# Performance work log

Hardware: AMD Instinct MI355X
Metric: run time of the kernel (lower is better)

The kernel has to match this reference:

```python
import jax, jax.numpy as jnp
import numpy as np

N_NODES = 50000
N_EDGES = 800000
D = 256
N_LAYERS = 3
BN_EPS = 1e-5


def setup_inputs() -> dict:
    key = jax.random.key(0)
    ks = jax.random.split(key, 7)
    x = jax.random.normal(ks[0], (N_NODES, D), dtype=jnp.float32)
    Wl = jax.random.normal(ks[1], (N_LAYERS, D, D), dtype=jnp.float32)
    bl = jax.random.normal(ks[2], (N_LAYERS, D), dtype=jnp.float32)
    Wr = jax.random.normal(ks[3], (N_LAYERS, D, D), dtype=jnp.float32)
    gamma = jax.random.uniform(ks[4], (N_LAYERS, D), dtype=jnp.float32)
    beta = jax.random.normal(ks[5], (N_LAYERS, D), dtype=jnp.float32)
    edge_index = jax.random.randint(ks[6], (2, N_EDGES), 0, N_NODES, dtype=jnp.int64)
    return {"x": x, "Wl": Wl, "bl": bl, "Wr": Wr, "gamma": gamma,
            "beta": beta, "edge_index": edge_index}


def reference(x, Wl, bl, Wr, gamma, beta, edge_index):
    """3-layer GNN: SAGEConv(mean) -> BatchNorm1d(train) -> ReLU per layer."""
    src = edge_index[0]
    dst = edge_index[1]
    n = x.shape[0]
    # In-degree (mean-aggregation denominator); clamp to avoid div-by-zero.
    deg = jax.ops.segment_sum(jnp.ones((src.shape[0],), dtype=x.dtype), dst,
                              num_segments=n)
    deg = jnp.maximum(deg, 1.0)[:, None]  # [N, 1]
    n_layers = Wl.shape[0]
    for i in range(n_layers):
        # --- SAGEConv: mean-aggregate neighbor messages, then linear ---
        agg = jax.ops.segment_sum(x[src], dst, num_segments=n) / deg  # [N, D]
        h = agg @ Wl[i] + bl[i] + x @ Wr[i]                           # [N, D]
        # --- BatchNorm1d (training mode: batch stats, biased variance) ---
        mu = jnp.mean(h, axis=0)
        var = jnp.mean(jnp.square(h - mu), axis=0)
        h = (h - mu) * jax.lax.rsqrt(var + BN_EPS) * gamma[i] + beta[i]
        # --- ReLU ---
        x = jax.nn.relu(h)
    return x
```

## Files before the change

### kernel.cpp

```cpp
#include <hip/hip_runtime.h>

#define N_NODES 50000
#define N_PAD   50176
#define N_EDGES 800000
#define DIM     256
#define KDIM    512
#define BN_EPS  1e-5f
#define SCAN_NB ((N_NODES + 1023) / 1024)

typedef __attribute__((ext_vector_type(8))) short short8;
typedef __attribute__((ext_vector_type(4))) float floatx4;

__device__ __forceinline__ float bf2f(unsigned short u) {
    return __uint_as_float(((unsigned int)u) << 16);
}
__device__ __forceinline__ unsigned short f2bf(float f) {
    unsigned int b = __float_as_uint(f);
    b = (b + 0x7FFF + ((b >> 16) & 1)) >> 16;
    return (unsigned short)b;
}

__device__ __forceinline__ void gload_lds16(const void* g, void* l) {
    __builtin_amdgcn_global_load_lds(
        (const __attribute__((address_space(1))) unsigned int*)g,
        (__attribute__((address_space(3))) unsigned int*)l, 16, 0, 0);
}


__global__ void k_deg_count(const int* __restrict__ dst, int* __restrict__ degi) {
    int e = blockIdx.x * blockDim.x + threadIdx.x;
    if (e < N_EDGES) atomicAdd(&degi[dst[e]], 1);
}

__global__ void k_scan1(const int* __restrict__ degi, int* __restrict__ off,
                        float* __restrict__ inv_deg, int* __restrict__ bsums) {
    __shared__ int buf[1024];
    int i = blockIdx.x * 1024 + threadIdx.x;
    int v = (i < N_NODES) ? degi[i] : 0;
    if (i < N_NODES) inv_deg[i] = 1.0f / (float)max(v, 1);
    buf[threadIdx.x] = v;
    __syncthreads();
    for (int s = 1; s < 1024; s <<= 1) {
        int t = (threadIdx.x >= s) ? buf[threadIdx.x - s] : 0;
        __syncthreads();
        buf[threadIdx.x] += t;
        __syncthreads();
    }
    if (i < N_NODES) off[i + 1] = buf[threadIdx.x];
    if (threadIdx.x == 1023) bsums[blockIdx.x] = buf[1023];
    if (i == 0) off[0] = 0;
}

__global__ void k_scan2(int* __restrict__ bsums) {
    int t = threadIdx.x;
    int orig = (t < SCAN_NB) ? bsums[t] : 0;
    int v = orig;
    for (int s = 1; s < 64; s <<= 1) {
        int u = __shfl_up(v, s, 64);
        if (t >= s) v += u;
    }
    if (t < SCAN_NB) bsums[t] = v - orig;
}

__global__ void k_scan3(int* __restrict__ off, const int* __restrict__ bsums) {
    int i = blockIdx.x * 1024 + threadIdx.x;
    if (i < N_NODES) off[i + 1] += bsums[blockIdx.x];
}

__global__ void k_fill(const int* __restrict__ src, const int* __restrict__ dst,
                       const int* __restrict__ off, int* __restrict__ cursor,
                       int* __restrict__ csr_src) {
    int e = blockIdx.x * blockDim.x + threadIdx.x;
    if (e < N_EDGES) {
        int d = dst[e];
        int pos = atomicAdd(&cursor[d], 1);
        csr_src[off[d] + pos] = src[e];
    }
}


__global__ void k_prep_w(const float* __restrict__ Wl, const float* __restrict__ Wr,
                         unsigned short* __restrict__ Wcat) {
    int gid = blockIdx.x * blockDim.x + threadIdx.x;
    if (gid >= 3 * DIM * KDIM) return;
    int k = gid & (KDIM - 1);
    int n = (gid >> 9) & (DIM - 1);
    int l = gid >> 17;
    float v = (k < DIM) ? Wl[(size_t)l * DIM * DIM + (size_t)k * DIM + n]
                        : Wr[(size_t)l * DIM * DIM + (size_t)(k - DIM) * DIM + n];
    Wcat[gid] = f2bf(v);
}


__global__ void k_x2bf(const float* __restrict__ x, unsigned short* __restrict__ Acat) {
    size_t i = (size_t)blockIdx.x * blockDim.x + threadIdx.x;
    if (i >= (size_t)N_NODES * (DIM / 4)) return;
    int node = (int)(i >> 6);
    int c = ((int)i & 63) * 4;
    float4 v = ((const float4*)x)[i];
    ushort4 o; o.x = f2bf(v.x); o.y = f2bf(v.y); o.z = f2bf(v.z); o.w = f2bf(v.w);
    *(ushort4*)&Acat[(size_t)node * KDIM + DIM + c] = o;
}


__device__ __forceinline__ void addv(float* a, uint4 v) {
    unsigned int w[4] = {v.x, v.y, v.z, v.w};
    #pragma unroll
    for (int q = 0; q < 4; ++q) {
        a[2 * q + 0] += bf2f((unsigned short)(w[q] & 0xFFFF));
        a[2 * q + 1] += bf2f((unsigned short)(w[q] >> 16));
    }
}

__global__ __launch_bounds__(256) void k_aggregate(
        const unsigned short* __restrict__ Acat_x,
        const int* __restrict__ off,
        const int* __restrict__ csr_src,
        const float* __restrict__ inv_deg,
        unsigned short* __restrict__ Acat_agg) {
    int gid = blockIdx.x * blockDim.x + threadIdx.x;
    int node = gid >> 5;
    int lane = threadIdx.x & 31;
    if (node >= N_NODES) return;
    int beg = off[node], end = off[node + 1];
    float a[8];
    #pragma unroll
    for (int q = 0; q < 8; ++q) a[q] = 0.f;
    const unsigned short* xb = Acat_x + DIM + lane * 8;

    int e = beg;
    for (; e + 8 <= end; e += 8) {
        uint4 v0 = *(const uint4*)(xb + (size_t)csr_src[e + 0] * KDIM);
        uint4 v1 = *(const uint4*)(xb + (size_t)csr_src[e + 1] * KDIM);
        uint4 v2 = *(const uint4*)(xb + (size_t)csr_src[e + 2] * KDIM);
        uint4 v3 = *(const uint4*)(xb + (size_t)csr_src[e + 3] * KDIM);
        uint4 v4 = *(const uint4*)(xb + (size_t)csr_src[e + 4] * KDIM);
        uint4 v5 = *(const uint4*)(xb + (size_t)csr_src[e + 5] * KDIM);
        uint4 v6 = *(const uint4*)(xb + (size_t)csr_src[e + 6] * KDIM);
        uint4 v7 = *(const uint4*)(xb + (size_t)csr_src[e + 7] * KDIM);
        addv(a, v0); addv(a, v1); addv(a, v2); addv(a, v3);
        addv(a, v4); addv(a, v5); addv(a, v6); addv(a, v7);
    }
    for (; e + 4 <= end; e += 4) {
        uint4 v0 = *(const uint4*)(xb + (size_t)csr_src[e + 0] * KDIM);
        uint4 v1 = *(const uint4*)(xb + (size_t)csr_src[e + 1] * KDIM);
        uint4 v2 = *(const uint4*)(xb + (size_t)csr_src[e + 2] * KDIM);
        uint4 v3 = *(const uint4*)(xb + (size_t)csr_src[e + 3] * KDIM);
        addv(a, v0); addv(a, v1); addv(a, v2); addv(a, v3);
    }
    for (; e < end; ++e) {
        uint4 v = *(const uint4*)(xb + (size_t)csr_src[e] * KDIM);
        addv(a, v);
    }

    float inv = inv_deg[node];
    unsigned int w[4];
    #pragma unroll
    for (int q = 0; q < 4; ++q)
        w[q] = (unsigned int)f2bf(a[2 * q] * inv) |
               ((unsigned int)f2bf(a[2 * q + 1] * inv) << 16);
    uint4 o; o.x = w[0]; o.y = w[1]; o.z = w[2]; o.w = w[3];
    *(uint4*)&Acat_agg[(size_t)node * KDIM + lane * 8] = o;
}


__global__ __launch_bounds__(256) void k_gemm_mfma(
        const unsigned short* __restrict__ A,
        const unsigned short* __restrict__ Bt,
        const float* __restrict__ bias, unsigned short* __restrict__ H,
        float* __restrict__ ssum, float* __restrict__ ssq) {
    __shared__ __align__(16) short Alds[2][128 * 32];
    __shared__ __align__(16) short Blds[2][128 * 32];
    int tid = threadIdx.x;
    int wid = tid >> 6;
    int lane = tid & 63;
    int wm = wid >> 1, wn = wid & 1;
    int brow = blockIdx.x * 128;
    int bcol = blockIdx.y * 128;

    floatx4 acc[4][4];
    #pragma unroll
    for (int i = 0; i < 4; ++i)
        #pragma unroll
        for (int j = 0; j < 4; ++j) acc[i][j] = (floatx4){0.f, 0.f, 0.f, 0.f};

    int st_r0 = (lane >> 2);
    int st_s  = lane & 3;
    int rb = lane & 15;
    int k16r = lane >> 4;

    auto stage = [&](int buf, int kt) {
        int k0 = kt * 32;
        #pragma unroll
        for (int q = 0; q < 2; ++q) {
            int c = wid * 2 + q;
            int r = c * 16 + st_r0;
            int k16 = (st_s - (r >> 1)) & 3;
            gload_lds16(A + (size_t)(brow + r) * KDIM + k0 + k16 * 8, &Alds[buf][c * 512]);
            gload_lds16(Bt + (size_t)(bcol + r) * KDIM + k0 + k16 * 8, &Blds[buf][c * 512]);
        }
    };

    stage(0, 0);
    __syncthreads();
    int cur = 0;
    for (int kt = 0; kt < KDIM / 32; ++kt) {
        if (kt + 1 < KDIM / 32) stage(cur ^ 1, kt + 1);

        short8 af[4], bfr[4];
        #pragma unroll
        for (int i = 0; i < 4; ++i) {
            int ra = wm * 64 + i * 16 + rb;
            int sa = (k16r + (ra >> 1)) & 3;
            af[i] = *(const short8*)&Alds[cur][ra * 32 + sa * 8];
            int rc = wn * 64 + i * 16 + rb;
            int sc = (k16r + (rc >> 1)) & 3;
            bfr[i] = *(const short8*)&Blds[cur][rc * 32 + sc * 8];
        }
        #pragma unroll
        for (int i = 0; i < 4; ++i)
            #pragma unroll
            for (int j = 0; j < 4; ++j)
                acc[i][j] = __builtin_amdgcn_mfma_f32_16x16x32_bf16(
                    af[i], bfr[j], acc[i][j], 0, 0, 0);
        __syncthreads();
        cur ^= 1;
    }

    int rg = lane >> 4;
    #pragma unroll
    for (int j = 0; j < 4; ++j) {
        int col = bcol + wn * 64 + j * 16 + rb;
        float bv = bias[col];
        float s = 0.f, s2 = 0.f;
        #pragma unroll
        for (int i = 0; i < 4; ++i) {
            #pragma unroll
            for (int q = 0; q < 4; ++q) {
                int row = brow + wm * 64 + i * 16 + rg * 4 + q;
                float o = acc[i][j][q] + bv;
                unsigned short hb = f2bf(o);
                if (row < N_NODES) {
                    H[(size_t)row * DIM + col] = hb;
                    float of = bf2f(hb);
                    s += of;
                    s2 = fmaf(of, of, s2);
                }
            }
        }
        s  += __shfl_xor(s, 16);
        s  += __shfl_xor(s, 32);
        s2 += __shfl_xor(s2, 16);
        s2 += __shfl_xor(s2, 32);
        if (rg == 0) {
            atomicAdd(&ssum[col], s);
            atomicAdd(&ssq[col], s2);
        }
    }
}


__global__ void k_norm_relu(const unsigned short* __restrict__ H,
                            const float* __restrict__ ssum,
                            const float* __restrict__ ssq,
                            const float* __restrict__ gamma,
                            const float* __restrict__ beta,
                            float* __restrict__ outF,
                            unsigned short* __restrict__ Acat, int last) {
    __shared__ float sc[DIM], sh[DIM];
    {
        int c = threadIdx.x;
        float mu  = ssum[c] * (1.0f / N_NODES);
        float var = ssq[c] * (1.0f / N_NODES) - mu * mu;
        float rstd = rsqrtf(var + BN_EPS);
        float s = rstd * gamma[c];
        sc[c] = s;
        sh[c] = beta[c] - mu * s;
    }
    __syncthreads();
    size_t total8 = (size_t)N_NODES * DIM / 8;
    for (size_t i = (size_t)blockIdx.x * blockDim.x + threadIdx.x; i < total8;
         i += (size_t)gridDim.x * blockDim.x) {
        uint4 raw = ((const uint4*)H)[i];
        int node = (int)(i >> 5);
        int c = ((int)i & 31) * 8;
        unsigned int w[4] = {raw.x, raw.y, raw.z, raw.w};
        float o[8];
        #pragma unroll
        for (int q = 0; q < 4; ++q) {
            float lo = bf2f((unsigned short)(w[q] & 0xFFFF));
            float hi = bf2f((unsigned short)(w[q] >> 16));
            o[q * 2 + 0] = fmaxf(fmaf(lo, sc[c + q * 2 + 0], sh[c + q * 2 + 0]), 0.f);
            o[q * 2 + 1] = fmaxf(fmaf(hi, sc[c + q * 2 + 1], sh[c + q * 2 + 1]), 0.f);
        }
        if (last) {
            float4 f0 = make_float4(o[0], o[1], o[2], o[3]);
            float4 f1 = make_float4(o[4], o[5], o[6], o[7]);
            *(float4*)(outF + (size_t)node * DIM + c)     = f0;
            *(float4*)(outF + (size_t)node * DIM + c + 4) = f1;
        } else {
            uint4 u;
            unsigned int uw[4];
            #pragma unroll
            for (int q = 0; q < 4; ++q)
                uw[q] = (unsigned int)f2bf(o[q * 2 + 0]) |
                        ((unsigned int)f2bf(o[q * 2 + 1]) << 16);
            u.x = uw[0]; u.y = uw[1]; u.z = uw[2]; u.w = uw[3];
            *(uint4*)&Acat[(size_t)node * KDIM + DIM + c] = u;
        }
    }
}


extern "C" void kernel_launch(void* const* d_in, const int* in_sizes, int n_in,
                              void* d_out, int out_size, void* d_ws, size_t ws_size,
                              hipStream_t stream) {
    const float* x0    = (const float*)d_in[0];
    const float* Wl    = (const float*)d_in[1];
    const float* bl    = (const float*)d_in[2];
    const float* Wr    = (const float*)d_in[3];
    const float* gamma = (const float*)d_in[4];
    const float* beta  = (const float*)d_in[5];
    const int*   ei    = (const int*)d_in[6];
    const int* e_src = ei;
    const int* e_dst = ei + N_EDGES;

    char* ws = (char*)d_ws;
    size_t off = 0;
    auto alloc = [&](size_t bytes) { char* p = ws + off; off = (off + bytes + 255) & ~(size_t)255; return p; };
    unsigned short* Acat = (unsigned short*)alloc((size_t)N_PAD * KDIM * 2);
    unsigned short* Hbuf = (unsigned short*)alloc((size_t)N_PAD * DIM * 2);
    unsigned short* Wcat = (unsigned short*)alloc((size_t)3 * DIM * KDIM * 2);
    int*   csr_src = (int*)alloc((size_t)N_EDGES * 4);
    int*   csr_off = (int*)alloc((size_t)(N_NODES + 1) * 4);
    int*   degi    = (int*)alloc((size_t)N_NODES * 4);
    int*   cursor  = (int*)alloc((size_t)N_NODES * 4);
    int*   bsums   = (int*)alloc((size_t)SCAN_NB * 4);
    float* inv_deg = (float*)alloc((size_t)N_NODES * 4);
    float* stats   = (float*)alloc((size_t)3 * 2 * DIM * 4);
    (void)ws_size;

    hipMemsetAsync(degi, 0, (size_t)N_NODES * 4, stream);
    hipMemsetAsync(cursor, 0, (size_t)N_NODES * 4, stream);
    hipMemsetAsync(stats, 0, (size_t)3 * 2 * DIM * 4, stream);

    int eb = (N_EDGES + 255) / 256;
    k_deg_count<<<eb, 256, 0, stream>>>(e_dst, degi);
    k_scan1<<<SCAN_NB, 1024, 0, stream>>>(degi, csr_off, inv_deg, bsums);
    k_scan2<<<1, 64, 0, stream>>>(bsums);
    k_scan3<<<SCAN_NB, 1024, 0, stream>>>(csr_off, bsums);
    k_fill<<<eb, 256, 0, stream>>>(e_src, e_dst, csr_off, cursor, csr_src);
    k_prep_w<<<(3 * DIM * KDIM + 255) / 256, 256, 0, stream>>>(Wl, Wr, Wcat);
    k_x2bf<<<(N_NODES * (DIM / 4) + 255) / 256, 256, 0, stream>>>(x0, Acat);

    for (int l = 0; l < 3; ++l) {
        float* ssum_l = stats + (size_t)l * 2 * DIM;
        float* ssq_l  = ssum_l + DIM;
        k_aggregate<<<(N_NODES * 32 + 255) / 256, 256, 0, stream>>>(
            Acat, csr_off, csr_src, inv_deg, Acat);
        k_gemm_mfma<<<dim3((N_NODES + 127) / 128, DIM / 128), 256, 0, stream>>>(
            Acat, Wcat + (size_t)l * DIM * KDIM, bl + (size_t)l * DIM, Hbuf, ssum_l, ssq_l);
        k_norm_relu<<<2048, 256, 0, stream>>>(Hbuf, ssum_l, ssq_l,
                                              gamma + (size_t)l * DIM, beta + (size_t)l * DIM,
                                              (float*)d_out, Acat, (l == 2) ? 1 : 0);
    }
}
```

Baseline: 584.9 us.

## Shrink GEMM row tile to 64 and add triple-buffered LDS pipeline

The node-feature GEMM now uses 64-row by 128-column tiles instead of 128x128, doubling the number of blocks. It also switches from double to triple buffering in LDS, issuing loads two K-steps ahead. Explicit vmcnt waits and raw s_barrier calls replace __syncthreads, so one barrier per iteration protects buffer reuse. This is meant to improve occupancy and overlap global-to-LDS loads with MFMA work, at the cost of re-reading the B tile more often and relying on hand-counted outstanding loads.

```diff
diff --git a/kernel.cpp b/kernel.cpp
--- a/kernel.cpp
+++ b/kernel.cpp
@@ -164,23 +164,25 @@
 }
 
 
+#define NT (KDIM / 32)
+
 __global__ __launch_bounds__(256) void k_gemm_mfma(
         const unsigned short* __restrict__ A,
         const unsigned short* __restrict__ Bt,
         const float* __restrict__ bias, unsigned short* __restrict__ H,
         float* __restrict__ ssum, float* __restrict__ ssq) {
-    __shared__ __align__(16) short Alds[2][128 * 32];
-    __shared__ __align__(16) short Blds[2][128 * 32];
+    __shared__ __align__(16) short Alds[3][64 * 32];
+    __shared__ __align__(16) short Blds[3][128 * 32];
     int tid = threadIdx.x;
     int wid = tid >> 6;
     int lane = tid & 63;
     int wm = wid >> 1, wn = wid & 1;
-    int brow = blockIdx.x * 128;
+    int brow = blockIdx.x * 64;
     int bcol = blockIdx.y * 128;
 
-    floatx4 acc[4][4];
-    #pragma unroll
-    for (int i = 0; i < 4; ++i)
+    floatx4 acc[2][4];
+    #pragma unroll
+    for (int i = 0; i < 2; ++i)
         #pragma unroll
         for (int j = 0; j < 4; ++j) acc[i][j] = (floatx4){0.f, 0.f, 0.f, 0.f};
 
@@ -191,40 +193,61 @@
 
     auto stage = [&](int buf, int kt) {
         int k0 = kt * 32;
+        {
+            int r = wid * 16 + st_r0;
+            int k16 = (st_s - (r >> 1)) & 3;
+            gload_lds16(A + (size_t)(brow + r) * KDIM + k0 + k16 * 8,
+                        &Alds[buf][wid * 512]);
+        }
         #pragma unroll
         for (int q = 0; q < 2; ++q) {
             int c = wid * 2 + q;
             int r = c * 16 + st_r0;
             int k16 = (st_s - (r >> 1)) & 3;
-            gload_lds16(A + (size_t)(brow + r) * KDIM + k0 + k16 * 8, &Alds[buf][c * 512]);
-            gload_lds16(Bt + (size_t)(bcol + r) * KDIM + k0 + k16 * 8, &Blds[buf][c * 512]);
+            gload_lds16(Bt + (size_t)(bcol + r) * KDIM + k0 + k16 * 8,
+                        &Blds[buf][c * 512]);
         }
     };
 
     stage(0, 0);
-    __syncthreads();
-    int cur = 0;
-    for (int kt = 0; kt < KDIM / 32; ++kt) {
-        if (kt + 1 < KDIM / 32) stage(cur ^ 1, kt + 1);
-
-        short8 af[4], bfr[4];
-        #pragma unroll
-        for (int i = 0; i < 4; ++i) {
-            int ra = wm * 64 + i * 16 + rb;
+    stage(1, 1);
+    asm volatile("s_waitcnt vmcnt(3)" ::: "memory");
+    __builtin_amdgcn_s_barrier();
+    __builtin_amdgcn_sched_barrier(0);
+
+    for (int kt = 0; kt < NT; ++kt) {
+        int cur = kt % 3;
+        if (kt + 2 < NT) stage((kt + 2) % 3, kt + 2);
+
+        short8 af[2], bfr[4];
+        #pragma unroll
+        for (int i = 0; i < 2; ++i) {
+            int ra = wm * 32 + i * 16 + rb;
             int sa = (k16r + (ra >> 1)) & 3;
             af[i] = *(const short8*)&Alds[cur][ra * 32 + sa * 8];
-            int rc = wn * 64 + i * 16 + rb;
+        }
+        #pragma unroll
+        for (int j = 0; j < 4; ++j) {
+            int rc = wn * 64 + j * 16 + rb;
             int sc = (k16r + (rc >> 1)) & 3;
-            bfr[i] = *(const short8*)&Blds[cur][rc * 32 + sc * 8];
-        }
-        #pragma unroll
-        for (int i = 0; i < 4; ++i)
+            bfr[j] = *(const short8*)&Blds[cur][rc * 32 + sc * 8];
+        }
+        #pragma unroll
+        for (int i = 0; i < 2; ++i)
             #pragma unroll
             for (int j = 0; j < 4; ++j)
                 acc[i][j] = __builtin_amdgcn_mfma_f32_16x16x32_bf16(
                     af[i], bfr[j], acc[i][j], 0, 0, 0);
-        __syncthreads();
-        cur ^= 1;
+
+        if (kt + 2 < NT) {
+            asm volatile("s_waitcnt vmcnt(3)" ::: "memory");
+        } else if (kt + 1 < NT) {
+            asm volatile("s_waitcnt vmcnt(0)" ::: "memory");
+        }
+        if (kt + 1 < NT) {
+            __builtin_amdgcn_s_barrier();
+            __builtin_amdgcn_sched_barrier(0);
+        }
     }
 
     int rg = lane >> 4;
@@ -234,10 +257,10 @@
         float bv = bias[col];
         float s = 0.f, s2 = 0.f;
         #pragma unroll
-        for (int i = 0; i < 4; ++i) {
+        for (int i = 0; i < 2; ++i) {
             #pragma unroll
             for (int q = 0; q < 4; ++q) {
-                int row = brow + wm * 64 + i * 16 + rg * 4 + q;
+                int row = brow + wm * 32 + i * 16 + rg * 4 + q;
                 float o = acc[i][j][q] + bv;
                 unsigned short hb = f2bf(o);
                 if (row < N_NODES) {
@@ -358,7 +381,7 @@
         float* ssq_l  = ssum_l + DIM;
         k_aggregate<<<(N_NODES * 32 + 255) / 256, 256, 0, stream>>>(
             Acat, csr_off, csr_src, inv_deg, Acat);
-        k_gemm_mfma<<<dim3((N_NODES + 127) / 128, DIM / 128), 256, 0, stream>>>(
+        k_gemm_mfma<<<dim3(N_PAD / 64, DIM / 128), 256, 0, stream>>>(
             Acat, Wcat + (size_t)l * DIM * KDIM, bl + (size_t)l * DIM, Hbuf, ssum_l, ssq_l);
         k_norm_relu<<<2048, 256, 0, stream>>>(Hbuf, ssum_l, ssq_l,
                                               gamma + (size_t)l * DIM, beta + (size_t)l * DIM,
```

Result: slower. 680.9 us (+16.4%).
